# Optimization experiments

Measured on AMD Instinct MI355X. Metric: run time of the kernel, lower is better.

Reference implementation:

```python
import jax, jax.numpy as jnp
import numpy as np

FIELD_DIMS = [256] * 8          # 8 fields, 2048 total features
N_FACTORS = 64
BATCH = 8192
INIT_STD = 0.01


def setup_inputs() -> dict:
    key = jax.random.key(0)
    k_x, k_v = jax.random.split(key)
    n_features = sum(FIELD_DIMS)
    n_fields = len(FIELD_DIMS)
    x = jax.random.normal(k_x, (BATCH, n_features), dtype=jnp.float32)
    # Parameters initialized as in FFMtorchNN.initialize()
    b = jnp.zeros((1,), dtype=jnp.float32)
    w = jnp.zeros((n_features, 1), dtype=jnp.float32)
    V = INIT_STD * jax.random.normal(k_v, (n_features, n_fields, N_FACTORS), dtype=jnp.float32)
    # feat2field[i] = field index of feature i
    feat2field = jnp.asarray(np.repeat(np.arange(n_fields), FIELD_DIMS), dtype=jnp.int32)
    return {"x": x, "b": b, "w": w, "V": V, "feat2field": feat2field}


def reference(x, b, w, V, feat2field):
    # Linear term: sum(x @ w, dim=1) -> [B]
    total_linear = (x @ w)[:, 0]

    n_fields = V.shape[1]
    # One-hot field membership of each feature: E [F, n_fields]
    E = jax.nn.one_hot(feat2field, n_fields, dtype=x.dtype)
    # M[b, s, t, l] = sum_{i in field s} x[b,i] * V[i, t, l]
    M = jnp.einsum('bi,is,itl->bstl', x, E, V)

    # Full ordered-pair bilinear sum: sum_{i,j} x_i x_j <V[i, f(j)], V[j, f(i)]>
    full = jnp.einsum('bstl,btsl->b', M, M)
    # Self terms (i == j): x_i^2 * ||V[i, f(i)]||^2
    V_self = jnp.take_along_axis(V, feat2field[:, None, None].astype(jnp.int32), axis=1)[:, 0, :]  # [F, L]
    q = jnp.einsum('bi,i->b', x * x, jnp.sum(V_self * V_self, axis=-1))

    # Original: total_inter = sum_{i<j} 0.5 * <t_i, t_j>  ==  0.25 * (full - q)
    total_inter = 0.25 * (full - q)

    y_pred = b[0] + total_linear + total_inter  # [B]
    return y_pred
```

## Files before the change

kernel.cpp:

```cpp
#include <hip/hip_runtime.h>

#define BATCH  8192
#define NFEAT  2048
#define NFIELD 8
#define NFACT  64
#define FDIM   256
#define NPAIR  36

typedef short short8v __attribute__((ext_vector_type(8)));
typedef __bf16 bf16x8 __attribute__((ext_vector_type(8)));
typedef float f32x4 __attribute__((ext_vector_type(4)));

__device__ inline unsigned short f2bf(float f) {
    unsigned int u = __float_as_uint(f);
    unsigned int r = u + 0x7FFF + ((u >> 16) & 1);
    return (unsigned short)(r >> 16);
}
__device__ inline float bf2f(unsigned short h) {
    return __uint_as_float(((unsigned int)h) << 16);
}
__device__ inline f32x4 mfma16(bf16x8 a, bf16x8 b, f32x4 c) {
    return __builtin_amdgcn_mfma_f32_16x16x32_bf16(a, b, c, 0, 0, 0);
}

__global__ void sv_kernel(const float* __restrict__ V, const int* __restrict__ f2f,
                          float* __restrict__ sv) {
    int i = blockIdx.x * blockDim.x + threadIdx.x;
    if (i >= NFEAT) return;
    int f = f2f[i];
    const float* vp = V + (size_t)i * (NFIELD * NFACT) + (size_t)f * NFACT;
    float s = 0.f;
#pragma unroll
    for (int l = 0; l < NFACT; l += 4) {
        float4 v = *reinterpret_cast<const float4*>(vp + l);
        s += v.x * v.x + v.y * v.y + v.z * v.z + v.w * v.w;
    }
    sv[i] = s;
}

__global__ void init_out(const float* __restrict__ bptr, float* __restrict__ out) {
    int i = blockIdx.x * blockDim.x + threadIdx.x;
    if (i < BATCH) out[i] = bptr[0];
}

__global__ void convert_v(const float* __restrict__ V,
                          unsigned short* __restrict__ vh, unsigned short* __restrict__ vl) {
    const int tid = blockIdx.x * 256 + threadIdx.x;
    const int lane = tid & 63;
    const int ct = (tid >> 6) & 3;
    const int kc = (tid >> 8) & 7;
    const int t  = (tid >> 11) & 7;
    const int s  = tid >> 14;
    const int l  = ct * 16 + (lane & 15);
    const int i0 = s * 256 + kc * 32 + (lane >> 4) * 8;
    short8v hv, lv;
#pragma unroll
    for (int e = 0; e < 8; ++e) {
        float v = V[(size_t)(i0 + e) * (NFIELD * NFACT) + t * NFACT + l];
        unsigned short h = f2bf(v);
        hv[e] = (short)h;
        lv[e] = (short)f2bf(v - bf2f(h));
    }
    *reinterpret_cast<short8v*>(vh + (size_t)tid * 8) = hv;
    *reinterpret_cast<short8v*>(vl + (size_t)tid * 8) = lv;
}

__global__ void convert_x_fused(const float* __restrict__ x, const float* __restrict__ w,
                                const float* __restrict__ sv,
                                unsigned short* __restrict__ xh, unsigned short* __restrict__ xl,
                                float* __restrict__ out) {
    const int tid = blockIdx.x * 256 + threadIdx.x;
    const int lane = tid & 63;
    const int rt = (tid >> 6) & 7;
    const int kc = (tid >> 9) & 7;
    const int s  = (tid >> 12) & 7;
    const int rb = tid >> 15;
    const int row = rb * 128 + rt * 16 + (lane & 15);
    const int col = s * 256 + kc * 32 + (lane >> 4) * 8;

    const float* xp = x + (size_t)row * NFEAT + col;
    float4 a  = *reinterpret_cast<const float4*>(xp);
    float4 b4 = *reinterpret_cast<const float4*>(xp + 4);
    float4 w0 = *reinterpret_cast<const float4*>(w + col);
    float4 w1 = *reinterpret_cast<const float4*>(w + col + 4);
    float4 s0 = *reinterpret_cast<const float4*>(sv + col);
    float4 s1 = *reinterpret_cast<const float4*>(sv + col + 4);

    float xs[8] = {a.x, a.y, a.z, a.w, b4.x, b4.y, b4.z, b4.w};
    float wsv[8] = {w0.x, w0.y, w0.z, w0.w, w1.x, w1.y, w1.z, w1.w};
    float ss[8] = {s0.x, s0.y, s0.z, s0.w, s1.x, s1.y, s1.z, s1.w};

    short8v hv, lv;
    float lin = 0.f, q = 0.f;
#pragma unroll
    for (int e = 0; e < 8; ++e) {
        float v = xs[e];
        unsigned short h = f2bf(v);
        float hf = bf2f(h);
        hv[e] = (short)h;
        lv[e] = (short)f2bf(v - hf);
        lin += v * wsv[e];
        q   += v * v * ss[e];
    }
    *reinterpret_cast<short8v*>(xh + (size_t)tid * 8) = hv;
    *reinterpret_cast<short8v*>(xl + (size_t)tid * 8) = lv;

    float c = lin - 0.25f * q;
    c += __shfl_xor(c, 16, 64);
    c += __shfl_xor(c, 32, 64);
    if ((lane >> 4) == 0) atomicAdd(&out[row], c);
}

__global__ __launch_bounds__(256, 3) void pair_mfma(
    const unsigned short* __restrict__ xh, const unsigned short* __restrict__ xl,
    const unsigned short* __restrict__ vh, const unsigned short* __restrict__ vl,
    float* __restrict__ out) {
    __shared__ unsigned short lds[24576];

    const int tile = blockIdx.x;
    int p = blockIdx.y;
    int s = 0;
    while (p >= NFIELD - s) { p -= NFIELD - s; ++s; }
    const int t = s + p;
    const bool diag = (s == t);

    const int tid = threadIdx.x, lane = tid & 63, wid = tid >> 6;

    f32x4 accA[2][4] = {};
    f32x4 accB[2][4] = {};

    const unsigned short* xsrc = (wid & 1) ? xl : xh;
    const unsigned short* vsrc = (wid & 1) ? vl : vh;
    const int f     = (wid < 2) ? s : t;
    const int vpair = (wid < 2) ? (s * 8 + t) : (t * 8 + s);
    const int xdst  = wid * 4096;
    const int vdst  = 16384 + wid * 2048;
    const bool active = !(diag && wid >= 2);

    for (int kc = 0; kc < 8; ++kc) {
        short8v xr[8], vr[4];
        if (active) {
            size_t xb = ((size_t)((tile * 8 + f) * 8 + kc)) * 4096 + lane * 8;
#pragma unroll
            for (int rt = 0; rt < 8; ++rt)
                xr[rt] = *reinterpret_cast<const short8v*>(xsrc + xb + rt * 512);
            size_t vb = ((size_t)(vpair * 8 + kc)) * 2048 + lane * 8;
#pragma unroll
            for (int ct = 0; ct < 4; ++ct)
                vr[ct] = *reinterpret_cast<const short8v*>(vsrc + vb + ct * 512);
        }
        __syncthreads();
        if (active) {
#pragma unroll
            for (int rt = 0; rt < 8; ++rt)
                *reinterpret_cast<short8v*>(&lds[xdst + rt * 512 + lane * 8]) = xr[rt];
#pragma unroll
            for (int ct = 0; ct < 4; ++ct)
                *reinterpret_cast<short8v*>(&lds[vdst + ct * 512 + lane * 8]) = vr[ct];
        }
        __syncthreads();

        const int rt0 = wid * 2, rt1 = rt0 + 1;
        bf16x8 ah0 = *reinterpret_cast<const bf16x8*>(&lds[0     + rt0 * 512 + lane * 8]);
        bf16x8 ah1 = *reinterpret_cast<const bf16x8*>(&lds[0     + rt1 * 512 + lane * 8]);
        bf16x8 al0 = *reinterpret_cast<const bf16x8*>(&lds[4096  + rt0 * 512 + lane * 8]);
        bf16x8 al1 = *reinterpret_cast<const bf16x8*>(&lds[4096  + rt1 * 512 + lane * 8]);
#pragma unroll
        for (int ct = 0; ct < 4; ++ct) {
            bf16x8 bh = *reinterpret_cast<const bf16x8*>(&lds[16384 + ct * 512 + lane * 8]);
            bf16x8 bl = *reinterpret_cast<const bf16x8*>(&lds[18432 + ct * 512 + lane * 8]);
            accA[0][ct] = mfma16(ah0, bh, accA[0][ct]);
            accA[0][ct] = mfma16(ah0, bl, accA[0][ct]);
            accA[0][ct] = mfma16(al0, bh, accA[0][ct]);
            accA[1][ct] = mfma16(ah1, bh, accA[1][ct]);
            accA[1][ct] = mfma16(ah1, bl, accA[1][ct]);
            accA[1][ct] = mfma16(al1, bh, accA[1][ct]);
        }
        if (!diag) {
            bf16x8 ch0 = *reinterpret_cast<const bf16x8*>(&lds[8192  + rt0 * 512 + lane * 8]);
            bf16x8 ch1 = *reinterpret_cast<const bf16x8*>(&lds[8192  + rt1 * 512 + lane * 8]);
            bf16x8 cl0 = *reinterpret_cast<const bf16x8*>(&lds[12288 + rt0 * 512 + lane * 8]);
            bf16x8 cl1 = *reinterpret_cast<const bf16x8*>(&lds[12288 + rt1 * 512 + lane * 8]);
#pragma unroll
            for (int ct = 0; ct < 4; ++ct) {
                bf16x8 bh = *reinterpret_cast<const bf16x8*>(&lds[20480 + ct * 512 + lane * 8]);
                bf16x8 bl = *reinterpret_cast<const bf16x8*>(&lds[22528 + ct * 512 + lane * 8]);
                accB[0][ct] = mfma16(ch0, bh, accB[0][ct]);
                accB[0][ct] = mfma16(ch0, bl, accB[0][ct]);
                accB[0][ct] = mfma16(cl0, bh, accB[0][ct]);
                accB[1][ct] = mfma16(ch1, bh, accB[1][ct]);
                accB[1][ct] = mfma16(ch1, bl, accB[1][ct]);
                accB[1][ct] = mfma16(cl1, bh, accB[1][ct]);
            }
        }
    }

    const float scale = diag ? 0.25f : 0.5f;
#pragma unroll
    for (int rti = 0; rti < 2; ++rti) {
#pragma unroll
        for (int r = 0; r < 4; ++r) {
            float v = 0.f;
#pragma unroll
            for (int ct = 0; ct < 4; ++ct)
                v += accA[rti][ct][r] * (diag ? accA[rti][ct][r] : accB[rti][ct][r]);
            v += __shfl_xor(v, 1, 64);
            v += __shfl_xor(v, 2, 64);
            v += __shfl_xor(v, 4, 64);
            v += __shfl_xor(v, 8, 64);
            if ((lane & 15) == 0) {
                int row = tile * 128 + (wid * 2 + rti) * 16 + (lane >> 4) * 4 + r;
                atomicAdd(&out[row], scale * v);
            }
        }
    }
}

#define BM 64
#define KC 64
#define XPAD 4

__global__ void base_kernel(const float* __restrict__ x, const float* __restrict__ bptr,
                            const float* __restrict__ w, const float* __restrict__ sv,
                            float* __restrict__ out) {
    const int row = blockIdx.x;
    const int tid = threadIdx.x;
    const float* xr = x + (size_t)row * NFEAT;
    float lin = 0.f, q = 0.f;
#pragma unroll
    for (int j = 0; j < 2; ++j) {
        int idx = j * 1024 + tid * 4;
        float4 xv = *reinterpret_cast<const float4*>(xr + idx);
        float4 wv = *reinterpret_cast<const float4*>(w + idx);
        float4 sq = *reinterpret_cast<const float4*>(sv + idx);
        lin += xv.x * wv.x + xv.y * wv.y + xv.z * wv.z + xv.w * wv.w;
        q   += xv.x * xv.x * sq.x + xv.y * xv.y * sq.y
             + xv.z * xv.z * sq.z + xv.w * xv.w * sq.w;
    }
#pragma unroll
    for (int off = 32; off >= 1; off >>= 1) {
        lin += __shfl_down(lin, off, 64);
        q   += __shfl_down(q, off, 64);
    }
    __shared__ float slin[4], sq4[4];
    const int wave = tid >> 6;
    if ((tid & 63) == 0) { slin[wave] = lin; sq4[wave] = q; }
    __syncthreads();
    if (tid == 0) {
        float L = slin[0] + slin[1] + slin[2] + slin[3];
        float Q = sq4[0] + sq4[1] + sq4[2] + sq4[3];
        out[row] = bptr[0] + L - 0.25f * Q;
    }
}

__global__ __launch_bounds__(256) void pair_kernel(const float* __restrict__ x,
                                                   const float* __restrict__ V,
                                                   float* __restrict__ out) {
    __shared__ float Xs[BM][KC + XPAD];
    __shared__ float Xt[BM][KC + XPAD];
    __shared__ float Vs[KC][NFACT];
    __shared__ float Vt[KC][NFACT];

    const int tile = blockIdx.x;
    int p = blockIdx.y;
    int s = 0;
    while (p >= NFIELD - s) { p -= NFIELD - s; ++s; }
    const int t = s + p;
    const bool diag = (s == t);

    const int tid  = threadIdx.x;
    const int lgrp = tid & 15;
    const int rgrp = tid >> 4;
    const int l0 = lgrp * 4;
    const int r0 = rgrp * 4;
    const int rowBase = tile * BM;

    float accA[4][4] = {};
    float accB[4][4] = {};

    for (int kc = 0; kc < FDIM; kc += KC) {
        __syncthreads();
#pragma unroll
        for (int it = 0; it < 4; ++it) {
            int rr = (tid >> 4) + it * 16;
            const float* gx = x + (size_t)(rowBase + rr) * NFEAT + s * FDIM + kc + (tid & 15) * 4;
            *reinterpret_cast<float4*>(&Xs[rr][(tid & 15) * 4]) =
                *reinterpret_cast<const float4*>(gx);
            if (!diag) {
                const float* gx2 = x + (size_t)(rowBase + rr) * NFEAT + t * FDIM + kc + (tid & 15) * 4;
                *reinterpret_cast<float4*>(&Xt[rr][(tid & 15) * 4]) =
                    *reinterpret_cast<const float4*>(gx2);
            }
        }
#pragma unroll
        for (int it = 0; it < 4; ++it) {
            int kk = (tid >> 4) + it * 16;
            const float* gv = V + (size_t)(s * FDIM + kc + kk) * (NFIELD * NFACT) + t * NFACT + (tid & 15) * 4;
            *reinterpret_cast<float4*>(&Vs[kk][(tid & 15) * 4]) =
                *reinterpret_cast<const float4*>(gv);
            if (!diag) {
                const float* gv2 = V + (size_t)(t * FDIM + kc + kk) * (NFIELD * NFACT) + s * NFACT + (tid & 15) * 4;
                *reinterpret_cast<float4*>(&Vt[kk][(tid & 15) * 4]) =
                    *reinterpret_cast<const float4*>(gv2);
            }
        }
        __syncthreads();

        for (int k = 0; k < KC; k += 4) {
            float xa[4][4], va[4][4];
#pragma unroll
            for (int r = 0; r < 4; ++r) {
                float4 v = *reinterpret_cast<const float4*>(&Xs[r0 + r][k]);
                xa[r][0] = v.x; xa[r][1] = v.y; xa[r][2] = v.z; xa[r][3] = v.w;
            }
#pragma unroll
            for (int kk = 0; kk < 4; ++kk) {
                float4 v = *reinterpret_cast<const float4*>(&Vs[k + kk][l0]);
                va[kk][0] = v.x; va[kk][1] = v.y; va[kk][2] = v.z; va[kk][3] = v.w;
            }
#pragma unroll
            for (int kk = 0; kk < 4; ++kk)
#pragma unroll
                for (int r = 0; r < 4; ++r)
#pragma unroll
                    for (int c = 0; c < 4; ++c)
                        accA[r][c] = fmaf(xa[r][kk], va[kk][c], accA[r][c]);

            if (!diag) {
                float xb[4][4], vb[4][4];
#pragma unroll
                for (int r = 0; r < 4; ++r) {
                    float4 v = *reinterpret_cast<const float4*>(&Xt[r0 + r][k]);
                    xb[r][0] = v.x; xb[r][1] = v.y; xb[r][2] = v.z; xb[r][3] = v.w;
                }
#pragma unroll
                for (int kk = 0; kk < 4; ++kk) {
                    float4 v = *reinterpret_cast<const float4*>(&Vt[k + kk][l0]);
                    vb[kk][0] = v.x; vb[kk][1] = v.y; vb[kk][2] = v.z; vb[kk][3] = v.w;
                }
#pragma unroll
                for (int kk = 0; kk < 4; ++kk)
#pragma unroll
                    for (int r = 0; r < 4; ++r)
#pragma unroll
                        for (int c = 0; c < 4; ++c)
                            accB[r][c] = fmaf(xb[r][kk], vb[kk][c], accB[r][c]);
            }
        }
    }

    float pr[4];
#pragma unroll
    for (int r = 0; r < 4; ++r) {
        float d = 0.f;
#pragma unroll
        for (int c = 0; c < 4; ++c)
            d += accA[r][c] * (diag ? accA[r][c] : accB[r][c]);
        pr[r] = d;
    }
#pragma unroll
    for (int off = 1; off < 16; off <<= 1) {
#pragma unroll
        for (int r = 0; r < 4; ++r)
            pr[r] += __shfl_xor(pr[r], off, 64);
    }
    if (lgrp == 0) {
        const float scale = diag ? 0.25f : 0.5f;
#pragma unroll
        for (int r = 0; r < 4; ++r)
            atomicAdd(&out[rowBase + r0 + r], scale * pr[r]);
    }
}

extern "C" void kernel_launch(void* const* d_in, const int* in_sizes, int n_in,
                              void* d_out, int out_size, void* d_ws, size_t ws_size,
                              hipStream_t stream) {
    const float* x   = (const float*)d_in[0];
    const float* b   = (const float*)d_in[1];
    const float* w   = (const float*)d_in[2];
    const float* V   = (const float*)d_in[3];
    const int*   f2f = (const int*)d_in[4];
    float* out = (float*)d_out;

    const size_t SZ_XH = 33554432;
    const size_t SZ_VH = 2097152;
    const size_t NEED  = 2 * SZ_XH + 2 * SZ_VH + NFEAT * sizeof(float);

    if (ws_size >= NEED) {
        char* ws = (char*)d_ws;
        unsigned short* xh  = (unsigned short*)ws;
        unsigned short* xl  = (unsigned short*)(ws + SZ_XH);
        unsigned short* vhp = (unsigned short*)(ws + 2 * SZ_XH);
        unsigned short* vlp = (unsigned short*)(ws + 2 * SZ_XH + SZ_VH);
        float* sv = (float*)(ws + 2 * SZ_XH + 2 * SZ_VH);

        sv_kernel<<<(NFEAT + 255) / 256, 256, 0, stream>>>(V, f2f, sv);
        init_out<<<(BATCH + 255) / 256, 256, 0, stream>>>(b, out);
        convert_v<<<131072 / 256, 256, 0, stream>>>(V, vhp, vlp);
        convert_x_fused<<<2097152 / 256, 256, 0, stream>>>(x, w, sv, xh, xl, out);
        dim3 grid(BATCH / 128, NPAIR);
        pair_mfma<<<grid, 256, 0, stream>>>(xh, xl, vhp, vlp, out);
    } else {
        float* sv = (float*)d_ws;
        sv_kernel<<<(NFEAT + 255) / 256, 256, 0, stream>>>(V, f2f, sv);
        base_kernel<<<BATCH, 256, 0, stream>>>(x, b, w, sv, out);
        dim3 grid(BATCH / BM, NPAIR);
        pair_kernel<<<grid, 256, 0, stream>>>(x, V, out);
    }
}
```

Baseline: 180.6 us.

## Coalesce x conversion via LDS tile, drop init kernel, load MFMA operands directly

The x conversion kernel now reads full 16-row tiles with coalesced float4 loads through shared memory. It also computes the linear and self terms per row with wave reductions and writes bias plus result directly, which removes the init_out kernel and the atomics. The pair kernel drops its LDS staging and the two barriers per k-step, loading pre-swizzled bf16 fragments straight from global memory into registers. It also uses a 1D grid swizzled so that consecutive blocks share the same field pair. In exchange, x fragments are re-read from global or L2 by every wave with no LDS reuse, and the occupancy hint is removed.

```diff
diff --git a/kernel.cpp b/kernel.cpp
--- a/kernel.cpp
+++ b/kernel.cpp
@@ -36,11 +36,6 @@
         s += v.x * v.x + v.y * v.y + v.z * v.z + v.w * v.w;
     }
     sv[i] = s;
-}
-
-__global__ void init_out(const float* __restrict__ bptr, float* __restrict__ out) {
-    int i = blockIdx.x * blockDim.x + threadIdx.x;
-    if (i < BATCH) out[i] = bptr[0];
 }
 
 __global__ void convert_v(const float* __restrict__ V,
@@ -65,132 +60,145 @@
     *reinterpret_cast<short8v*>(vl + (size_t)tid * 8) = lv;
 }
 
-__global__ void convert_x_fused(const float* __restrict__ x, const float* __restrict__ w,
-                                const float* __restrict__ sv,
-                                unsigned short* __restrict__ xh, unsigned short* __restrict__ xl,
-                                float* __restrict__ out) {
-    const int tid = blockIdx.x * 256 + threadIdx.x;
+__global__ __launch_bounds__(256) void convert_x2(
+    const float* __restrict__ x, const float* __restrict__ w,
+    const float* __restrict__ sv, const float* __restrict__ bptr,
+    unsigned short* __restrict__ xh, unsigned short* __restrict__ xl,
+    float* __restrict__ out) {
+    __shared__ float tile[16][268];
+
+    const int blk  = blockIdx.x;
+    const int rb   = blk >> 3;
+    const int rt   = blk & 7;
+    const int row0 = blk * 16;
+    const int tid  = threadIdx.x;
     const int lane = tid & 63;
-    const int rt = (tid >> 6) & 7;
-    const int kc = (tid >> 9) & 7;
-    const int s  = (tid >> 12) & 7;
-    const int rb = tid >> 15;
-    const int row = rb * 128 + rt * 16 + (lane & 15);
-    const int col = s * 256 + kc * 32 + (lane >> 4) * 8;
-
-    const float* xp = x + (size_t)row * NFEAT + col;
-    float4 a  = *reinterpret_cast<const float4*>(xp);
-    float4 b4 = *reinterpret_cast<const float4*>(xp + 4);
-    float4 w0 = *reinterpret_cast<const float4*>(w + col);
-    float4 w1 = *reinterpret_cast<const float4*>(w + col + 4);
-    float4 s0 = *reinterpret_cast<const float4*>(sv + col);
-    float4 s1 = *reinterpret_cast<const float4*>(sv + col + 4);
-
-    float xs[8] = {a.x, a.y, a.z, a.w, b4.x, b4.y, b4.z, b4.w};
-    float wsv[8] = {w0.x, w0.y, w0.z, w0.w, w1.x, w1.y, w1.z, w1.w};
-    float ss[8] = {s0.x, s0.y, s0.z, s0.w, s1.x, s1.y, s1.z, s1.w};
-
-    short8v hv, lv;
-    float lin = 0.f, q = 0.f;
-#pragma unroll
-    for (int e = 0; e < 8; ++e) {
-        float v = xs[e];
-        unsigned short h = f2bf(v);
-        float hf = bf2f(h);
-        hv[e] = (short)h;
-        lv[e] = (short)f2bf(v - hf);
-        lin += v * wsv[e];
-        q   += v * v * ss[e];
-    }
-    *reinterpret_cast<short8v*>(xh + (size_t)tid * 8) = hv;
-    *reinterpret_cast<short8v*>(xl + (size_t)tid * 8) = lv;
-
-    float c = lin - 0.25f * q;
-    c += __shfl_xor(c, 16, 64);
-    c += __shfl_xor(c, 32, 64);
-    if ((lane >> 4) == 0) atomicAdd(&out[row], c);
-}
-
-__global__ __launch_bounds__(256, 3) void pair_mfma(
+    const int wv   = tid >> 6;
+
+    float lin[4] = {0.f, 0.f, 0.f, 0.f};
+    float qq[4]  = {0.f, 0.f, 0.f, 0.f};
+
+    for (int s = 0; s < 8; ++s) {
+        const int col = s * 256 + lane * 4;
+        float4 w4  = *reinterpret_cast<const float4*>(w + col);
+        float4 sv4 = *reinterpret_cast<const float4*>(sv + col);
+        __syncthreads();
+#pragma unroll
+        for (int p = 0; p < 4; ++p) {
+            int r = p * 4 + wv;
+            float4 v = *reinterpret_cast<const float4*>(
+                x + (size_t)(row0 + r) * NFEAT + col);
+            *reinterpret_cast<float4*>(&tile[r][lane * 4]) = v;
+            lin[p] += v.x * w4.x + v.y * w4.y + v.z * w4.z + v.w * w4.w;
+            qq[p]  += v.x * v.x * sv4.x + v.y * v.y * sv4.y
+                    + v.z * v.z * sv4.z + v.w * v.w * sv4.w;
+        }
+        __syncthreads();
+#pragma unroll
+        for (int half = 0; half < 2; ++half) {
+            const int kc = half * 4 + wv;
+            const int r  = lane & 15;
+            const int k0 = kc * 32 + (lane >> 4) * 8;
+            float4 a = *reinterpret_cast<const float4*>(&tile[r][k0]);
+            float4 b = *reinterpret_cast<const float4*>(&tile[r][k0 + 4]);
+            float vs[8] = {a.x, a.y, a.z, a.w, b.x, b.y, b.z, b.w};
+            short8v hv, lv;
+#pragma unroll
+            for (int e = 0; e < 8; ++e) {
+                unsigned short h = f2bf(vs[e]);
+                hv[e] = (short)h;
+                lv[e] = (short)f2bf(vs[e] - bf2f(h));
+            }
+            size_t off = ((((size_t)(rb * 8 + s) * 8 + kc) * 8 + rt) * 64 + lane) * 8;
+            *reinterpret_cast<short8v*>(xh + off) = hv;
+            *reinterpret_cast<short8v*>(xl + off) = lv;
+        }
+    }
+
+#pragma unroll
+    for (int off = 1; off < 64; off <<= 1) {
+#pragma unroll
+        for (int p = 0; p < 4; ++p) {
+            lin[p] += __shfl_xor(lin[p], off, 64);
+            qq[p]  += __shfl_xor(qq[p], off, 64);
+        }
+    }
+    if (lane == 0) {
+        float b0 = bptr[0];
+#pragma unroll
+        for (int p = 0; p < 4; ++p)
+            out[row0 + p * 4 + wv] = b0 + lin[p] - 0.25f * qq[p];
+    }
+}
+
+__global__ __launch_bounds__(256) void pair_mfma2(
     const unsigned short* __restrict__ xh, const unsigned short* __restrict__ xl,
     const unsigned short* __restrict__ vh, const unsigned short* __restrict__ vl,
     float* __restrict__ out) {
-    __shared__ unsigned short lds[24576];
-
-    const int tile = blockIdx.x;
-    int p = blockIdx.y;
-    int s = 0;
+    const int id  = blockIdx.x;
+    const int swz = (id & 7) * 288 + (id >> 3);
+    const int pairIdx = swz >> 6;
+    const int tile    = swz & 63;
+
+    int p = pairIdx, s = 0;
     while (p >= NFIELD - s) { p -= NFIELD - s; ++s; }
     const int t = s + p;
     const bool diag = (s == t);
 
     const int tid = threadIdx.x, lane = tid & 63, wid = tid >> 6;
+    const int rt0 = wid * 2, rt1 = rt0 + 1;
 
     f32x4 accA[2][4] = {};
     f32x4 accB[2][4] = {};
 
-    const unsigned short* xsrc = (wid & 1) ? xl : xh;
-    const unsigned short* vsrc = (wid & 1) ? vl : vh;
-    const int f     = (wid < 2) ? s : t;
-    const int vpair = (wid < 2) ? (s * 8 + t) : (t * 8 + s);
-    const int xdst  = wid * 4096;
-    const int vdst  = 16384 + wid * 2048;
-    const bool active = !(diag && wid >= 2);
+    const size_t laneOff = (size_t)lane * 8;
+    const size_t xbS = ((size_t)(tile * 8 + s) * 8) * 4096 + laneOff;
+    const size_t xbT = ((size_t)(tile * 8 + t) * 8) * 4096 + laneOff;
+    const size_t vbA = ((size_t)(s * 8 + t) * 8) * 2048 + laneOff;
+    const size_t vbB = ((size_t)(t * 8 + s) * 8) * 2048 + laneOff;
 
     for (int kc = 0; kc < 8; ++kc) {
-        short8v xr[8], vr[4];
-        if (active) {
-            size_t xb = ((size_t)((tile * 8 + f) * 8 + kc)) * 4096 + lane * 8;
-#pragma unroll
-            for (int rt = 0; rt < 8; ++rt)
-                xr[rt] = *reinterpret_cast<const short8v*>(xsrc + xb + rt * 512);
-            size_t vb = ((size_t)(vpair * 8 + kc)) * 2048 + lane * 8;
-#pragma unroll
-            for (int ct = 0; ct < 4; ++ct)
-                vr[ct] = *reinterpret_cast<const short8v*>(vsrc + vb + ct * 512);
-        }
-        __syncthreads();
-        if (active) {
-#pragma unroll
-            for (int rt = 0; rt < 8; ++rt)
-                *reinterpret_cast<short8v*>(&lds[xdst + rt * 512 + lane * 8]) = xr[rt];
-#pragma unroll
-            for (int ct = 0; ct < 4; ++ct)
-                *reinterpret_cast<short8v*>(&lds[vdst + ct * 512 + lane * 8]) = vr[ct];
-        }
-        __syncthreads();
-
-        const int rt0 = wid * 2, rt1 = rt0 + 1;
-        bf16x8 ah0 = *reinterpret_cast<const bf16x8*>(&lds[0     + rt0 * 512 + lane * 8]);
-        bf16x8 ah1 = *reinterpret_cast<const bf16x8*>(&lds[0     + rt1 * 512 + lane * 8]);
-        bf16x8 al0 = *reinterpret_cast<const bf16x8*>(&lds[4096  + rt0 * 512 + lane * 8]);
-        bf16x8 al1 = *reinterpret_cast<const bf16x8*>(&lds[4096  + rt1 * 512 + lane * 8]);
+        const size_t xo = (size_t)kc * 4096;
+        const size_t vo = (size_t)kc * 2048;
+
+        bf16x8 ah0 = *reinterpret_cast<const bf16x8*>(xh + xbS + xo + rt0 * 512);
+        bf16x8 ah1 = *reinterpret_cast<const bf16x8*>(xh + xbS + xo + rt1 * 512);
+        bf16x8 al0 = *reinterpret_cast<const bf16x8*>(xl + xbS + xo + rt0 * 512);
+        bf16x8 al1 = *reinterpret_cast<const bf16x8*>(xl + xbS + xo + rt1 * 512);
+        bf16x8 vah[4], val[4];
 #pragma unroll
         for (int ct = 0; ct < 4; ++ct) {
-            bf16x8 bh = *reinterpret_cast<const bf16x8*>(&lds[16384 + ct * 512 + lane * 8]);
-            bf16x8 bl = *reinterpret_cast<const bf16x8*>(&lds[18432 + ct * 512 + lane * 8]);
-            accA[0][ct] = mfma16(ah0, bh, accA[0][ct]);
-            accA[0][ct] = mfma16(ah0, bl, accA[0][ct]);
-            accA[0][ct] = mfma16(al0, bh, accA[0][ct]);
-            accA[1][ct] = mfma16(ah1, bh, accA[1][ct]);
-            accA[1][ct] = mfma16(ah1, bl, accA[1][ct]);
-            accA[1][ct] = mfma16(al1, bh, accA[1][ct]);
+            vah[ct] = *reinterpret_cast<const bf16x8*>(vh + vbA + vo + ct * 512);
+            val[ct] = *reinterpret_cast<const bf16x8*>(vl + vbA + vo + ct * 512);
+        }
+#pragma unroll
+        for (int ct = 0; ct < 4; ++ct) {
+            accA[0][ct] = mfma16(ah0, vah[ct], accA[0][ct]);
+            accA[0][ct] = mfma16(ah0, val[ct], accA[0][ct]);
+            accA[0][ct] = mfma16(al0, vah[ct], accA[0][ct]);
+            accA[1][ct] = mfma16(ah1, vah[ct], accA[1][ct]);
+            accA[1][ct] = mfma16(ah1, val[ct], accA[1][ct]);
+            accA[1][ct] = mfma16(al1, vah[ct], accA[1][ct]);
         }
         if (!diag) {
-            bf16x8 ch0 = *reinterpret_cast<const bf16x8*>(&lds[8192  + rt0 * 512 + lane * 8]);
-            bf16x8 ch1 = *reinterpret_cast<const bf16x8*>(&lds[8192  + rt1 * 512 + lane * 8]);
-            bf16x8 cl0 = *reinterpret_cast<const bf16x8*>(&lds[12288 + rt0 * 512 + lane * 8]);
-            bf16x8 cl1 = *reinterpret_cast<const bf16x8*>(&lds[12288 + rt1 * 512 + lane * 8]);
+            bf16x8 ch0 = *reinterpret_cast<const bf16x8*>(xh + xbT + xo + rt0 * 512);
+            bf16x8 ch1 = *reinterpret_cast<const bf16x8*>(xh + xbT + xo + rt1 * 512);
+            bf16x8 cl0 = *reinterpret_cast<const bf16x8*>(xl + xbT + xo + rt0 * 512);
+            bf16x8 cl1 = *reinterpret_cast<const bf16x8*>(xl + xbT + xo + rt1 * 512);
+            bf16x8 vbh[4], vbl[4];
 #pragma unroll
             for (int ct = 0; ct < 4; ++ct) {
-                bf16x8 bh = *reinterpret_cast<const bf16x8*>(&lds[20480 + ct * 512 + lane * 8]);
-                bf16x8 bl = *reinterpret_cast<const bf16x8*>(&lds[22528 + ct * 512 + lane * 8]);
-                accB[0][ct] = mfma16(ch0, bh, accB[0][ct]);
-                accB[0][ct] = mfma16(ch0, bl, accB[0][ct]);
-                accB[0][ct] = mfma16(cl0, bh, accB[0][ct]);
-                accB[1][ct] = mfma16(ch1, bh, accB[1][ct]);
-                accB[1][ct] = mfma16(ch1, bl, accB[1][ct]);
-                accB[1][ct] = mfma16(cl1, bh, accB[1][ct]);
+                vbh[ct] = *reinterpret_cast<const bf16x8*>(vh + vbB + vo + ct * 512);
+                vbl[ct] = *reinterpret_cast<const bf16x8*>(vl + vbB + vo + ct * 512);
+            }
+#pragma unroll
+            for (int ct = 0; ct < 4; ++ct) {
+                accB[0][ct] = mfma16(ch0, vbh[ct], accB[0][ct]);
+                accB[0][ct] = mfma16(ch0, vbl[ct], accB[0][ct]);
+                accB[0][ct] = mfma16(cl0, vbh[ct], accB[0][ct]);
+                accB[1][ct] = mfma16(ch1, vbh[ct], accB[1][ct]);
+                accB[1][ct] = mfma16(ch1, vbl[ct], accB[1][ct]);
+                accB[1][ct] = mfma16(cl1, vbh[ct], accB[1][ct]);
             }
         }
     }
@@ -388,18 +396,16 @@
 
     if (ws_size >= NEED) {
         char* ws = (char*)d_ws;
-        unsigned short* xh  = (unsigned short*)ws;
-        unsigned short* xl  = (unsigned short*)(ws + SZ_XH);
+        unsigned short* xhp = (unsigned short*)ws;
+        unsigned short* xlp = (unsigned short*)(ws + SZ_XH);
         unsigned short* vhp = (unsigned short*)(ws + 2 * SZ_XH);
         unsigned short* vlp = (unsigned short*)(ws + 2 * SZ_XH + SZ_VH);
         float* sv = (float*)(ws + 2 * SZ_XH + 2 * SZ_VH);
 
         sv_kernel<<<(NFEAT + 255) / 256, 256, 0, stream>>>(V, f2f, sv);
-        init_out<<<(BATCH + 255) / 256, 256, 0, stream>>>(b, out);
         convert_v<<<131072 / 256, 256, 0, stream>>>(V, vhp, vlp);
-        convert_x_fused<<<2097152 / 256, 256, 0, stream>>>(x, w, sv, xh, xl, out);
-        dim3 grid(BATCH / 128, NPAIR);
-        pair_mfma<<<grid, 256, 0, stream>>>(xh, xl, vhp, vlp, out);
+        convert_x2<<<BATCH / 16, 256, 0, stream>>>(x, w, sv, b, xhp, xlp, out);
+        pair_mfma2<<<64 * NPAIR, 256, 0, stream>>>(xhp, xlp, vhp, vlp, out);
     } else {
         float* sv = (float*)d_ws;
         sv_kernel<<<(NFEAT + 255) / 256, 256, 0, stream>>>(V, f2f, sv);
```

Result: slower. 212.2 us (+17.5%).

## Coalesce x conversion via LDS tile, prefetch next K chunk, remap pair grid

Applied to the files above, without the earlier changes.

The x conversion kernel now loads full contiguous 256-float row segments into an LDS tile. It computes the linear and self terms with one atomic per row per field, then writes the bf16 hi/lo MFMA layout from LDS, replacing strided per-thread float4 loads and many atomics. The pair MFMA kernel now issues global loads for chunk kc+1 into registers before computing on chunk kc, overlapping memory with MFMA. It also uses a 1D grid that groups blocks sharing a row tile so x tiles get L2 reuse. Register pressure rises under the 3-blocks-per-SM launch bound.

```diff
diff --git a/kernel.cpp b/kernel.cpp
--- a/kernel.cpp
+++ b/kernel.cpp
@@ -65,66 +65,90 @@
     *reinterpret_cast<short8v*>(vl + (size_t)tid * 8) = lv;
 }
 
-__global__ void convert_x_fused(const float* __restrict__ x, const float* __restrict__ w,
-                                const float* __restrict__ sv,
-                                unsigned short* __restrict__ xh, unsigned short* __restrict__ xl,
-                                float* __restrict__ out) {
-    const int tid = blockIdx.x * 256 + threadIdx.x;
+__global__ __launch_bounds__(256) void convert_x3(
+    const float* __restrict__ x, const float* __restrict__ w,
+    const float* __restrict__ sv,
+    unsigned short* __restrict__ xh, unsigned short* __restrict__ xl,
+    float* __restrict__ out) {
+    __shared__ float tile[16][260];
+
+    const int bid = blockIdx.x;
+    const int rb  = bid >> 6;
+    const int rt  = (bid >> 3) & 7;
+    const int s   = bid & 7;
+    const int row0 = rb * 128 + rt * 16;
+
+    const int tid  = threadIdx.x;
     const int lane = tid & 63;
-    const int rt = (tid >> 6) & 7;
-    const int kc = (tid >> 9) & 7;
-    const int s  = (tid >> 12) & 7;
-    const int rb = tid >> 15;
-    const int row = rb * 128 + rt * 16 + (lane & 15);
-    const int col = s * 256 + kc * 32 + (lane >> 4) * 8;
-
-    const float* xp = x + (size_t)row * NFEAT + col;
-    float4 a  = *reinterpret_cast<const float4*>(xp);
-    float4 b4 = *reinterpret_cast<const float4*>(xp + 4);
-    float4 w0 = *reinterpret_cast<const float4*>(w + col);
-    float4 w1 = *reinterpret_cast<const float4*>(w + col + 4);
-    float4 s0 = *reinterpret_cast<const float4*>(sv + col);
-    float4 s1 = *reinterpret_cast<const float4*>(sv + col + 4);
-
-    float xs[8] = {a.x, a.y, a.z, a.w, b4.x, b4.y, b4.z, b4.w};
-    float wsv[8] = {w0.x, w0.y, w0.z, w0.w, w1.x, w1.y, w1.z, w1.w};
-    float ss[8] = {s0.x, s0.y, s0.z, s0.w, s1.x, s1.y, s1.z, s1.w};
-
-    short8v hv, lv;
-    float lin = 0.f, q = 0.f;
-#pragma unroll
-    for (int e = 0; e < 8; ++e) {
-        float v = xs[e];
-        unsigned short h = f2bf(v);
-        float hf = bf2f(h);
-        hv[e] = (short)h;
-        lv[e] = (short)f2bf(v - hf);
-        lin += v * wsv[e];
-        q   += v * v * ss[e];
-    }
-    *reinterpret_cast<short8v*>(xh + (size_t)tid * 8) = hv;
-    *reinterpret_cast<short8v*>(xl + (size_t)tid * 8) = lv;
-
-    float c = lin - 0.25f * q;
-    c += __shfl_xor(c, 16, 64);
-    c += __shfl_xor(c, 32, 64);
-    if ((lane >> 4) == 0) atomicAdd(&out[row], c);
-}
-
-__global__ __launch_bounds__(256, 3) void pair_mfma(
+    const int wv   = tid >> 6;
+
+    const int col = s * 256 + lane * 4;
+    float4 w4  = *reinterpret_cast<const float4*>(w + col);
+    float4 sv4 = *reinterpret_cast<const float4*>(sv + col);
+
+    float lq[4];
+#pragma unroll
+    for (int p = 0; p < 4; ++p) {
+        const int r = wv * 4 + p;
+        float4 v = *reinterpret_cast<const float4*>(
+            x + (size_t)(row0 + r) * NFEAT + col);
+        *reinterpret_cast<float4*>(&tile[r][lane * 4]) = v;
+        float lin = v.x * w4.x + v.y * w4.y + v.z * w4.z + v.w * w4.w;
+        float q   = v.x * v.x * sv4.x + v.y * v.y * sv4.y
+                  + v.z * v.z * sv4.z + v.w * v.w * sv4.w;
+        lq[p] = lin - 0.25f * q;
+    }
+#pragma unroll
+    for (int off = 1; off < 64; off <<= 1)
+#pragma unroll
+        for (int p = 0; p < 4; ++p)
+            lq[p] += __shfl_xor(lq[p], off, 64);
+    if (lane == 0) {
+#pragma unroll
+        for (int p = 0; p < 4; ++p)
+            atomicAdd(&out[row0 + wv * 4 + p], lq[p]);
+    }
+
+    __syncthreads();
+
+#pragma unroll
+    for (int half = 0; half < 2; ++half) {
+        const int kc = half * 4 + wv;
+        const int r  = lane & 15;
+        const int k0 = kc * 32 + (lane >> 4) * 8;
+        float4 a = *reinterpret_cast<const float4*>(&tile[r][k0]);
+        float4 b = *reinterpret_cast<const float4*>(&tile[r][k0 + 4]);
+        float vs[8] = {a.x, a.y, a.z, a.w, b.x, b.y, b.z, b.w};
+        short8v hv, lv;
+#pragma unroll
+        for (int e = 0; e < 8; ++e) {
+            unsigned short h = f2bf(vs[e]);
+            hv[e] = (short)h;
+            lv[e] = (short)f2bf(vs[e] - bf2f(h));
+        }
+        size_t off = ((((size_t)(rb * 8 + s) * 8 + kc) * 8 + rt) * 64 + lane) * 8;
+        *reinterpret_cast<short8v*>(xh + off) = hv;
+        *reinterpret_cast<short8v*>(xl + off) = lv;
+    }
+}
+
+__global__ __launch_bounds__(256, 3) void pair_mfma3(
     const unsigned short* __restrict__ xh, const unsigned short* __restrict__ xl,
     const unsigned short* __restrict__ vh, const unsigned short* __restrict__ vl,
     float* __restrict__ out) {
     __shared__ unsigned short lds[24576];
 
-    const int tile = blockIdx.x;
-    int p = blockIdx.y;
+    const int id    = blockIdx.x;
+    const int local = id >> 3;
+    const int tile  = (id & 7) * 8 + local / 36;
+    int p = local % 36;
     int s = 0;
     while (p >= NFIELD - s) { p -= NFIELD - s; ++s; }
     const int t = s + p;
     const bool diag = (s == t);
 
     const int tid = threadIdx.x, lane = tid & 63, wid = tid >> 6;
+    const int rt0 = wid * 2, rt1 = rt0 + 1;
 
     f32x4 accA[2][4] = {};
     f32x4 accB[2][4] = {};
@@ -137,18 +161,20 @@
     const int vdst  = 16384 + wid * 2048;
     const bool active = !(diag && wid >= 2);
 
+    const size_t xbase = ((size_t)(tile * 8 + f) * 8) * 4096 + (size_t)lane * 8;
+    const size_t vbase = ((size_t)(vpair * 8)) * 2048 + (size_t)lane * 8;
+
+    short8v xr[8], vr[4];
+    if (active) {
+#pragma unroll
+        for (int rt = 0; rt < 8; ++rt)
+            xr[rt] = *reinterpret_cast<const short8v*>(xsrc + xbase + rt * 512);
+#pragma unroll
+        for (int ct = 0; ct < 4; ++ct)
+            vr[ct] = *reinterpret_cast<const short8v*>(vsrc + vbase + ct * 512);
+    }
+
     for (int kc = 0; kc < 8; ++kc) {
-        short8v xr[8], vr[4];
-        if (active) {
-            size_t xb = ((size_t)((tile * 8 + f) * 8 + kc)) * 4096 + lane * 8;
-#pragma unroll
-            for (int rt = 0; rt < 8; ++rt)
-                xr[rt] = *reinterpret_cast<const short8v*>(xsrc + xb + rt * 512);
-            size_t vb = ((size_t)(vpair * 8 + kc)) * 2048 + lane * 8;
-#pragma unroll
-            for (int ct = 0; ct < 4; ++ct)
-                vr[ct] = *reinterpret_cast<const short8v*>(vsrc + vb + ct * 512);
-        }
         __syncthreads();
         if (active) {
 #pragma unroll
@@ -160,7 +186,17 @@
         }
         __syncthreads();
 
-        const int rt0 = wid * 2, rt1 = rt0 + 1;
+        if (kc < 7 && active) {
+            const size_t xo = xbase + (size_t)(kc + 1) * 4096;
+            const size_t vo = vbase + (size_t)(kc + 1) * 2048;
+#pragma unroll
+            for (int rt = 0; rt < 8; ++rt)
+                xr[rt] = *reinterpret_cast<const short8v*>(xsrc + xo + rt * 512);
+#pragma unroll
+            for (int ct = 0; ct < 4; ++ct)
+                vr[ct] = *reinterpret_cast<const short8v*>(vsrc + vo + ct * 512);
+        }
+
         bf16x8 ah0 = *reinterpret_cast<const bf16x8*>(&lds[0     + rt0 * 512 + lane * 8]);
         bf16x8 ah1 = *reinterpret_cast<const bf16x8*>(&lds[0     + rt1 * 512 + lane * 8]);
         bf16x8 al0 = *reinterpret_cast<const bf16x8*>(&lds[4096  + rt0 * 512 + lane * 8]);
@@ -388,8 +424,8 @@
 
     if (ws_size >= NEED) {
         char* ws = (char*)d_ws;
-        unsigned short* xh  = (unsigned short*)ws;
-        unsigned short* xl  = (unsigned short*)(ws + SZ_XH);
+        unsigned short* xhp = (unsigned short*)ws;
+        unsigned short* xlp = (unsigned short*)(ws + SZ_XH);
         unsigned short* vhp = (unsigned short*)(ws + 2 * SZ_XH);
         unsigned short* vlp = (unsigned short*)(ws + 2 * SZ_XH + SZ_VH);
         float* sv = (float*)(ws + 2 * SZ_XH + 2 * SZ_VH);
@@ -397,9 +433,8 @@
         sv_kernel<<<(NFEAT + 255) / 256, 256, 0, stream>>>(V, f2f, sv);
         init_out<<<(BATCH + 255) / 256, 256, 0, stream>>>(b, out);
         convert_v<<<131072 / 256, 256, 0, stream>>>(V, vhp, vlp);
-        convert_x_fused<<<2097152 / 256, 256, 0, stream>>>(x, w, sv, xh, xl, out);
-        dim3 grid(BATCH / 128, NPAIR);
-        pair_mfma<<<grid, 256, 0, stream>>>(xh, xl, vhp, vlp, out);
+        convert_x3<<<4096, 256, 0, stream>>>(x, w, sv, xhp, xlp, out);
+        pair_mfma3<<<64 * NPAIR, 256, 0, stream>>>(xhp, xlp, vhp, vlp, out);
     } else {
         float* sv = (float*)d_ws;
         sv_kernel<<<(NFEAT + 255) / 256, 256, 0, stream>>>(V, f2f, sv);
```

New measurement: 178.9 us. No clear change (-0.9%).
